# Performance work log

Hardware: AMD Instinct MI355X
Metric: run time of the kernel (lower is better)

## Reference

```python
import jax, jax.numpy as jnp
import numpy as np
import math

B, SL, CH, HZ = 128, 5000, 12, 100
L, D, DFF, H, NC = 5, 1024, 4096, 16, 71
NI = CH * HZ  # 1200
S = SL // HZ  # 50


def setup_inputs() -> dict:
    key = jax.random.key(0)
    ks = jax.random.split(key, 12)
    r = lambda k, shp, sc: jax.random.normal(k, shp, jnp.float32) * sc
    return {
        'x': r(ks[0], (B, SL, CH), 1.0),
        'embed_w': r(ks[1], (NI, D), NI ** -0.5),
        'attn_w': r(ks[2], (L, 4, D, D), D ** -0.5),
        'attn_b': r(ks[3], (L, 4, D), 0.01),
        'ff_w1': r(ks[4], (L, D, DFF), D ** -0.5),
        'ff_b1': r(ks[5], (L, DFF), 0.01),
        'ff_w2': r(ks[6], (L, DFF, D), DFF ** -0.5),
        'ff_b2': r(ks[7], (L, D), 0.01),
        'ln_g': jnp.ones((L, 2, D)), 'ln_b': jnp.zeros((L, 2, D)),
        'fin_g': jnp.ones((D,)), 'fin_b': jnp.zeros((D,)),
        'cf_bn_g': jnp.ones((D,)), 'cf_bn_b': jnp.zeros((D,)),
        'cf_w': r(ks[8], (D, D), D ** -0.5), 'cf_b': r(ks[9], (D,), 0.01),
        'fc_bn_g': jnp.ones((D,)), 'fc_bn_b': jnp.zeros((D,)),
        'fc_w': r(ks[10], (D, NC), D ** -0.5), 'fc_b': r(ks[11], (NC,), 0.01),
    }


def _ln(t, g, b, eps=1e-6):
    # torch LayerNorm variant in source: unbiased std (ddof=1), divide by (std + eps)
    m = t.mean(-1, keepdims=True)
    s = jnp.std(t, axis=-1, ddof=1, keepdims=True)
    return g * (t - m) / (s + eps) + b


def reference(x, embed_w, attn_w, attn_b, ff_w1, ff_b1, ff_w2, ff_b2,
              ln_g, ln_b, fin_g, fin_b, cf_bn_g, cf_bn_b, cf_w, cf_b,
              fc_bn_g, fc_bn_b, fc_w, fc_b):
    Bx, SLx, CHx = x.shape
    Sx = SLx // HZ
    Dx = embed_w.shape[1]
    dk = Dx // H
    # Segmentation (fix): [B, SL, CH] -> [B, S, CH*HZ]; input embed (no bias)
    h = x.reshape(Bx, Sx, CHx * HZ) @ embed_w
    # Positional encoding (sin/cos, detached buffer)
    pos = jnp.arange(Sx, dtype=jnp.float32)[:, None]
    div = jnp.exp(jnp.arange(0, Dx, 2, dtype=jnp.float32) * (-math.log(10000.0) / Dx))
    pe = jnp.zeros((Sx, Dx), jnp.float32)
    pe = pe.at[:, 0::2].set(jnp.sin(pos * div)).at[:, 1::2].set(jnp.cos(pos * div))
    h = h + pe[None]
    # Pre-norm encoder stack (dropout = identity in eval)
    for i in range(attn_w.shape[0]):
        a = _ln(h, ln_g[i, 0], ln_b[i, 0])
        qkv = jnp.einsum('bsd,kde->kbse', a, attn_w[i, :3]) + attn_b[i, :3][:, None, None, :]
        q, k, v = [t.reshape(Bx, Sx, H, dk).transpose(0, 2, 1, 3) for t in qkv]  # bhsd
        sc = jnp.einsum('bhqd,bhkd->bhqk', q, k) / math.sqrt(dk)
        p = jax.nn.softmax(sc, axis=-1)
        o = jnp.einsum('bhqk,bhkd->bhqd', p, v).transpose(0, 2, 1, 3).reshape(Bx, Sx, Dx)
        h = h + o @ attn_w[i, 3] + attn_b[i, 3]
        a2 = _ln(h, ln_g[i, 1], ln_b[i, 1])
        h = h + jax.nn.relu(a2 @ ff_w1[i] + ff_b1[i]) @ ff_w2[i] + ff_b2[i]
    h = _ln(h, fin_g, fin_b)
    # LastPoolRNN(bidirectional=False): last time step
    pooled = h[:, -1, :]
    # BatchNorm1d in eval with running_mean=0, running_var=1
    inv = 1.0 / math.sqrt(1.0 + 1e-5)
    z = (pooled * inv) * cf_bn_g + cf_bn_b
    z = jax.nn.relu(z @ cf_w + cf_b)
    z = (z * inv) * fc_bn_g + fc_bn_b
    return z @ fc_w + fc_b
```

## Files before the change

### kernel.cpp

```cpp
#include <hip/hip_runtime.h>
#include <hip/hip_bf16.h>


typedef __attribute__((ext_vector_type(4))) float f32x4;
typedef __attribute__((ext_vector_type(8))) __bf16 bfvec8;

#define MTOT 6400
#define DMODEL 1024
#define KEMB 1216

__device__ __forceinline__ unsigned short f2bf(float x) {
    __hip_bfloat16 t = __float2bfloat16(x);
    return *reinterpret_cast<unsigned short*>(&t);
}

__device__ __forceinline__ void gl2lds16(const void* g, void* l) {
    __builtin_amdgcn_global_load_lds(
        (__attribute__((address_space(1))) void*)(g),
        (__attribute__((address_space(3))) void*)(l), 16, 0, 0);
}

__global__ __launch_bounds__(256) void tconv(const float* __restrict__ W,
                                             __hip_bfloat16* __restrict__ Wt,
                                             int K, int N, int Kpad) {
    __shared__ float t[32][33];
    const int n0 = blockIdx.x * 32, k0 = blockIdx.y * 32;
    const int tx = threadIdx.x, ty = threadIdx.y;
#pragma unroll
    for (int j = 0; j < 4; ++j) {
        int k = k0 + ty + j * 8, n = n0 + tx;
        float v = (k < K && n < N) ? W[(size_t)k * N + n] : 0.f;
        t[ty + j * 8][tx] = v;
    }
    __syncthreads();
#pragma unroll
    for (int j = 0; j < 4; ++j) {
        int n = n0 + ty + j * 8, k = k0 + tx;
        if (n < N && k < Kpad)
            ((unsigned short*)Wt)[(size_t)n * Kpad + k] = f2bf(t[tx][ty + j * 8]);
    }
}

__global__ __launch_bounds__(256) void xconv(const float* __restrict__ x,
                                             __hip_bfloat16* __restrict__ xb) {
    int q = blockIdx.x * 256 + threadIdx.x;
    if (q >= MTOT * (KEMB / 4)) return;
    int m = q / (KEMB / 4), kq = q - m * (KEMB / 4);
    ushort4 o;
    if (kq < 300) {
        float4 v = reinterpret_cast<const float4*>(x + (size_t)m * 1200)[kq];
        o.x = f2bf(v.x); o.y = f2bf(v.y); o.z = f2bf(v.z); o.w = f2bf(v.w);
    } else { o.x = 0; o.y = 0; o.z = 0; o.w = 0; }
    reinterpret_cast<ushort4*>(xb)[q] = o;
}

__global__ __launch_bounds__(256) void pe_kernel(float* __restrict__ pe) {
    int idx = blockIdx.x * 256 + threadIdx.x;
    if (idx >= 50 * 512) return;
    int s = idx >> 9, i = idx & 511;
    float dv = expf((float)(2 * i) * (-9.210340371976184f / 1024.0f));
    float a = (float)s * dv;
    pe[(s << 10) + 2 * i] = sinf(a);
    pe[(s << 10) + 2 * i + 1] = cosf(a);
}

template<int FLAGS>
__global__ __launch_bounds__(256) void gemm_bt(
                        const __hip_bfloat16* __restrict__ A,
                        const __hip_bfloat16* __restrict__ Bt,
                        float* __restrict__ outF, __hip_bfloat16* __restrict__ outB,
                        const float* __restrict__ bias, const float* __restrict__ res,
                        const float* __restrict__ pe,
                        const float* __restrict__ psg, const float* __restrict__ psb,
                        int M, int N, int K) {
    __shared__ short lds[16384];
    const int tid = threadIdx.x;
    const int w = tid >> 6, l = tid & 63;

    int bx, by;
    {
        const int nwg = gridDim.x * gridDim.y;
        const int wg  = blockIdx.y * gridDim.x + blockIdx.x;
        const int q = nwg >> 3, r = nwg & 7;
        const int xcd = wg & 7, pos = wg >> 3;
        const int nid = (xcd < r) ? xcd * (q + 1) + pos
                                  : r * (q + 1) + (xcd - r) * q + pos;
        by = nid / gridDim.x;
        bx = nid - by * gridDim.x;
    }
    const int row0 = by * 128, col0 = bx * 128;
    const int l15 = l & 15, kof = (l >> 4) << 3;
    const int wr = (w >> 1) << 6, wc = (w & 1) << 6;

    f32x4 acc[4][4];
#pragma unroll
    for (int m = 0; m < 4; ++m)
#pragma unroll
        for (int n = 0; n < 4; ++n) acc[m][n] = (f32x4){0.f, 0.f, 0.f, 0.f};

    int sr[4], sc[4];
#pragma unroll
    for (int c = 0; c < 4; ++c) {
        int e = c * 2048 + w * 512 + l * 8;
        int r = e >> 6;
        int cb = (e & 63) << 1;
        sr[c] = r;
        sc[c] = (cb ^ ((r & 7) << 4)) >> 1;
    }
    const int swz = (l15 & 7) << 4;

    for (int k0 = 0; k0 < K; k0 += 64) {
#pragma unroll
        for (int c = 0; c < 4; ++c)
            gl2lds16(A + (size_t)(row0 + sr[c]) * K + (k0 + sc[c]),
                     &lds[c * 2048 + w * 512]);
#pragma unroll
        for (int c = 0; c < 4; ++c)
            gl2lds16(Bt + (size_t)(col0 + sr[c]) * K + (k0 + sc[c]),
                     &lds[8192 + c * 2048 + w * 512]);
        __syncthreads();
#pragma unroll
        for (int kk = 0; kk < 64; kk += 32) {
            bfvec8 af[4], bfr[4];
#pragma unroll
            for (int m = 0; m < 4; ++m) {
                int r = wr + m * 16 + l15;
                af[m] = *(const bfvec8*)((const char*)lds + r * 128 + ((((kk + kof) << 1)) ^ swz));
            }
#pragma unroll
            for (int n = 0; n < 4; ++n) {
                int r = wc + n * 16 + l15;
                bfr[n] = *(const bfvec8*)((const char*)lds + 16384 + r * 128 + ((((kk + kof) << 1)) ^ swz));
            }
#pragma unroll
            for (int m = 0; m < 4; ++m)
#pragma unroll
                for (int n = 0; n < 4; ++n)
                    acc[m][n] = __builtin_amdgcn_mfma_f32_16x16x32_bf16(af[m], bfr[n], acc[m][n], 0, 0, 0);
        }
        __syncthreads();
    }

    const int rb = row0 + wr + ((l >> 4) << 2);
#pragma unroll
    for (int n = 0; n < 4; ++n) {
        const int cidx = col0 + wc + n * 16 + l15;
        float bv = 0.f, pg = 0.f, pb2 = 0.f;
        if constexpr (FLAGS & 1) bv = bias[cidx];
        if constexpr (FLAGS & 16) {
            pg = 0.99999500003749971f * psg[cidx];
            pb2 = psb[cidx];
        }
#pragma unroll
        for (int m = 0; m < 4; ++m) {
#pragma unroll
            for (int i = 0; i < 4; ++i) {
                int r = rb + m * 16 + i;
                float v = acc[m][n][i] + bv;
                if constexpr (FLAGS & 8) v += pe[(r % 50) * N + cidx];
                if constexpr (FLAGS & 4) v = fmaxf(v, 0.f);
                if constexpr (FLAGS & 2) v += res[(size_t)r * N + cidx];
                if constexpr (FLAGS & 16) v = v * pg + pb2;
                if constexpr (FLAGS & 32) ((unsigned short*)outB)[(size_t)r * N + cidx] = f2bf(v);
                else outF[(size_t)r * N + cidx] = v;
            }
        }
    }
}

__device__ __forceinline__ float wave_sum(float v) {
#pragma unroll
    for (int off = 32; off; off >>= 1) v += __shfl_down(v, off);
    return v;
}

__global__ __launch_bounds__(256) void ln_kernel(const float* __restrict__ h,
                                                 const float* __restrict__ g,
                                                 const float* __restrict__ b,
                                                 __hip_bfloat16* __restrict__ out) {
    const int row = blockIdx.x, tid = threadIdx.x;
    const float4 v = reinterpret_cast<const float4*>(h + (size_t)row * 1024)[tid];
    float s = v.x + v.y + v.z + v.w;
    float s2 = v.x * v.x + v.y * v.y + v.z * v.z + v.w * v.w;
    __shared__ float red[8];
    float ws1 = wave_sum(s), ws2 = wave_sum(s2);
    if ((tid & 63) == 0) { red[tid >> 6] = ws1; red[4 + (tid >> 6)] = ws2; }
    __syncthreads();
    float sum = red[0] + red[1] + red[2] + red[3];
    float sum2 = red[4] + red[5] + red[6] + red[7];
    float mean = sum * (1.f / 1024.f);
    float var = fmaxf(0.f, (sum2 - sum * mean) * (1.f / 1023.f));
    float inv = 1.f / (sqrtf(var) + 1e-6f);
    float4 gv = reinterpret_cast<const float4*>(g)[tid];
    float4 bv = reinterpret_cast<const float4*>(b)[tid];
    ushort4 o;
    o.x = f2bf(gv.x * (v.x - mean) * inv + bv.x);
    o.y = f2bf(gv.y * (v.y - mean) * inv + bv.y);
    o.z = f2bf(gv.z * (v.z - mean) * inv + bv.z);
    o.w = f2bf(gv.w * (v.w - mean) * inv + bv.w);
    reinterpret_cast<ushort4*>(out)[(size_t)row * 256 + tid] = o;
}

__global__ __launch_bounds__(256) void attn_k(const __hip_bfloat16* __restrict__ qkv,
                                              __hip_bfloat16* __restrict__ o) {
    __shared__ float Q[50][66];
    __shared__ float Kk[50][66];
    __shared__ float V[50][66];
    __shared__ float P[50][52];
    const int bid = blockIdx.x;
    const int b = bid >> 4, hh = bid & 15;
    const int tid = threadIdx.x;
    const size_t base0 = (size_t)(b * 50) * 3072 + hh * 64;
    for (int idx = tid; idx < 3200; idx += 256) {
        int s = idx >> 6, d = idx & 63;
        size_t p = base0 + (size_t)s * 3072 + d;
        Q[s][d] = __bfloat162float(qkv[p]);
        Kk[s][d] = __bfloat162float(qkv[p + 1024]);
        V[s][d] = __bfloat162float(qkv[p + 2048]);
    }
    __syncthreads();
    for (int e = tid; e < 2500; e += 256) {
        int i = e / 50, j = e - i * 50;
        float acc = 0.f;
#pragma unroll
        for (int d = 0; d < 64; ++d) acc += Q[i][d] * Kk[j][d];
        P[i][j] = acc * 0.125f;
    }
    __syncthreads();
    if (tid < 50) {
        float mx = -1e30f;
        for (int j = 0; j < 50; ++j) mx = fmaxf(mx, P[tid][j]);
        float sum = 0.f;
        for (int j = 0; j < 50; ++j) { float ev = __expf(P[tid][j] - mx); P[tid][j] = ev; sum += ev; }
        float is = 1.f / sum;
        for (int j = 0; j < 50; ++j) P[tid][j] *= is;
    }
    __syncthreads();
    for (int e = tid; e < 3200; e += 256) {
        int i = e >> 6, d = e & 63;
        float acc = 0.f;
#pragma unroll
        for (int j = 0; j < 50; ++j) acc += P[i][j] * V[j][d];
        o[(size_t)(b * 50 + i) * 1024 + hh * 64 + d] = __float2bfloat16(acc);
    }
}

__global__ __launch_bounds__(256) void pool_kernel(const float* __restrict__ h,
                                                   const float* __restrict__ fg,
                                                   const float* __restrict__ fb,
                                                   const float* __restrict__ cg,
                                                   const float* __restrict__ cb,
                                                   __hip_bfloat16* __restrict__ z) {
    const int bb = blockIdx.x, tid = threadIdx.x;
    const size_t row = (size_t)bb * 50 + 49;
    const float4 v = reinterpret_cast<const float4*>(h + row * 1024)[tid];
    float s = v.x + v.y + v.z + v.w;
    float s2 = v.x * v.x + v.y * v.y + v.z * v.z + v.w * v.w;
    __shared__ float red[8];
    float ws1 = wave_sum(s), ws2 = wave_sum(s2);
    if ((tid & 63) == 0) { red[tid >> 6] = ws1; red[4 + (tid >> 6)] = ws2; }
    __syncthreads();
    float sum = red[0] + red[1] + red[2] + red[3];
    float sum2 = red[4] + red[5] + red[6] + red[7];
    float mean = sum * (1.f / 1024.f);
    float var = fmaxf(0.f, (sum2 - sum * mean) * (1.f / 1023.f));
    float inv = 1.f / (sqrtf(var) + 1e-6f);
    const float INV = 0.99999500003749971f;
    float4 gv = reinterpret_cast<const float4*>(fg)[tid];
    float4 bv = reinterpret_cast<const float4*>(fb)[tid];
    float4 cgv = reinterpret_cast<const float4*>(cg)[tid];
    float4 cbv = reinterpret_cast<const float4*>(cb)[tid];
    ushort4 o;
    o.x = f2bf((gv.x * (v.x - mean) * inv + bv.x) * INV * cgv.x + cbv.x);
    o.y = f2bf((gv.y * (v.y - mean) * inv + bv.y) * INV * cgv.y + cbv.y);
    o.z = f2bf((gv.z * (v.z - mean) * inv + bv.z) * INV * cgv.z + cbv.z);
    o.w = f2bf((gv.w * (v.w - mean) * inv + bv.w) * INV * cgv.w + cbv.w);
    reinterpret_cast<ushort4*>(z)[(size_t)bb * 256 + tid] = o;
}

__global__ __launch_bounds__(128) void fc_kernel(const __hip_bfloat16* __restrict__ z3,
                                                 const float* __restrict__ fw,
                                                 const float* __restrict__ fbias,
                                                 float* __restrict__ out) {
    __shared__ float zr[1024];
    const int b = blockIdx.x, tid = threadIdx.x;
    for (int i = tid; i < 1024; i += 128) zr[i] = __bfloat162float(z3[(size_t)b * 1024 + i]);
    __syncthreads();
    if (tid < 71) {
        float acc = 0.f;
        for (int k = 0; k < 1024; ++k) acc += zr[k] * fw[k * 71 + tid];
        out[b * 71 + tid] = acc + fbias[tid];
    }
}

extern "C" void kernel_launch(void* const* d_in, const int* in_sizes, int n_in,
                              void* d_out, int out_size, void* d_ws, size_t ws_size,
                              hipStream_t stream) {
    const float* x       = (const float*)d_in[0];
    const float* embed_w = (const float*)d_in[1];
    const float* attn_w  = (const float*)d_in[2];
    const float* attn_b  = (const float*)d_in[3];
    const float* ff_w1   = (const float*)d_in[4];
    const float* ff_b1   = (const float*)d_in[5];
    const float* ff_w2   = (const float*)d_in[6];
    const float* ff_b2   = (const float*)d_in[7];
    const float* ln_g    = (const float*)d_in[8];
    const float* ln_b    = (const float*)d_in[9];
    const float* fin_g   = (const float*)d_in[10];
    const float* fin_b   = (const float*)d_in[11];
    const float* cf_bn_g = (const float*)d_in[12];
    const float* cf_bn_b = (const float*)d_in[13];
    const float* cf_w    = (const float*)d_in[14];
    const float* cf_b    = (const float*)d_in[15];
    const float* fc_bn_g = (const float*)d_in[16];
    const float* fc_bn_b = (const float*)d_in[17];
    const float* fc_w    = (const float*)d_in[18];
    const float* fc_b    = (const float*)d_in[19];

    char* ws = (char*)d_ws;
    size_t off = 0;
    auto alloc = [&](size_t bytes) { void* p = ws + off; off += (bytes + 255) & ~(size_t)255; return p; };

    __hip_bfloat16* wbuf = (__hip_bfloat16*)alloc((size_t)12582912 * 2);
    float*          h    = (float*)alloc((size_t)MTOT * DMODEL * 4);
    __hip_bfloat16* abuf = (__hip_bfloat16*)alloc((size_t)MTOT * DMODEL * 2);
    __hip_bfloat16* big  = (__hip_bfloat16*)alloc((size_t)MTOT * 4096 * 2);
    float*          pe   = (float*)alloc((size_t)50 * 1024 * 4);
    __hip_bfloat16* zbuf = (__hip_bfloat16*)alloc((size_t)128 * 1024 * 2);
    __hip_bfloat16* z3   = (__hip_bfloat16*)alloc((size_t)128 * 1024 * 2);

    __hip_bfloat16* qkvT = wbuf;
    __hip_bfloat16* projT = wbuf + (size_t)3072 * 1024;
    __hip_bfloat16* ff1T = wbuf + (size_t)4096 * 1024;
    __hip_bfloat16* ff2T = wbuf + (size_t)8192 * 1024;

    const dim3 tb(32, 8);

    xconv<<<(MTOT * (KEMB / 4) + 255) / 256, 256, 0, stream>>>(x, big);
    pe_kernel<<<100, 256, 0, stream>>>(pe);
    tconv<<<dim3(32, 38), tb, 0, stream>>>(embed_w, wbuf, 1200, 1024, KEMB);
    gemm_bt<8><<<dim3(8, 50), 256, 0, stream>>>(big, wbuf, h, nullptr,
        nullptr, nullptr, pe, nullptr, nullptr, MTOT, DMODEL, KEMB);

    for (int i = 0; i < 5; ++i) {
        for (int k = 0; k < 3; ++k)
            tconv<<<dim3(32, 32), tb, 0, stream>>>(attn_w + ((size_t)i * 4 + k) * 1048576,
                                                   qkvT + (size_t)k * 1048576, 1024, 1024, 1024);
        tconv<<<dim3(32, 32), tb, 0, stream>>>(attn_w + ((size_t)i * 4 + 3) * 1048576,
                                               projT, 1024, 1024, 1024);
        tconv<<<dim3(128, 32), tb, 0, stream>>>(ff_w1 + (size_t)i * 4194304, ff1T, 1024, 4096, 1024);
        tconv<<<dim3(32, 128), tb, 0, stream>>>(ff_w2 + (size_t)i * 4194304, ff2T, 4096, 1024, 4096);

        ln_kernel<<<MTOT, 256, 0, stream>>>(h, ln_g + (size_t)i * 2048, ln_b + (size_t)i * 2048, abuf);
        gemm_bt<33><<<dim3(24, 50), 256, 0, stream>>>(abuf, qkvT, nullptr, big,
            attn_b + (size_t)i * 4096, nullptr, nullptr, nullptr, nullptr, MTOT, 3072, 1024);
        attn_k<<<2048, 256, 0, stream>>>(big, abuf);
        gemm_bt<3><<<dim3(8, 50), 256, 0, stream>>>(abuf, projT, h, nullptr,
            attn_b + (size_t)i * 4096 + 3072, h, nullptr, nullptr, nullptr, MTOT, DMODEL, 1024);
        ln_kernel<<<MTOT, 256, 0, stream>>>(h, ln_g + (size_t)i * 2048 + 1024,
                                            ln_b + (size_t)i * 2048 + 1024, abuf);
        gemm_bt<37><<<dim3(32, 50), 256, 0, stream>>>(abuf, ff1T, nullptr, big,
            ff_b1 + (size_t)i * 4096, nullptr, nullptr, nullptr, nullptr, MTOT, 4096, 1024);
        gemm_bt<3><<<dim3(8, 50), 256, 0, stream>>>(big, ff2T, h, nullptr,
            ff_b2 + (size_t)i * 1024, h, nullptr, nullptr, nullptr, MTOT, DMODEL, 4096);
    }

    pool_kernel<<<128, 256, 0, stream>>>(h, fin_g, fin_b, cf_bn_g, cf_bn_b, zbuf);
    tconv<<<dim3(32, 32), tb, 0, stream>>>(cf_w, wbuf, 1024, 1024, 1024);
    gemm_bt<53><<<dim3(8, 1), 256, 0, stream>>>(zbuf, wbuf, nullptr, z3,
        cf_b, nullptr, nullptr, fc_bn_g, fc_bn_b, 128, 1024, 1024);
    fc_kernel<<<128, 128, 0, stream>>>(z3, fc_w, fc_b, (float*)d_out);

    (void)in_sizes; (void)n_in; (void)out_size; (void)ws_size;
}
```

Before: 2.168 ms.

## Rewrite attention with bf16 MFMA per wave and batch attention weight transposes

Replaces the scalar fp32 LDS attention kernel with one where each wave handles one head. QK^T and PV run on 16x16x32 bf16 MFMA instructions, softmax uses register shuffles, and P and V are staged in padded LDS. The four per-layer attention weight transposes are merged into one launch using a z grid dimension, which cuts launch overhead. P is now rounded to bf16 before the PV product, so there is a small precision change.

New measurement: 1.895 ms. -12.6%, faster.

```diff
diff --git a/kernel.cpp b/kernel.cpp
--- a/kernel.cpp
+++ b/kernel.cpp
@@ -22,14 +22,16 @@
 
 __global__ __launch_bounds__(256) void tconv(const float* __restrict__ W,
                                              __hip_bfloat16* __restrict__ Wt,
-                                             int K, int N, int Kpad) {
+                                             int K, int N, int Kpad, size_t zoff) {
     __shared__ float t[32][33];
+    const float* Wz = W + (size_t)blockIdx.z * zoff;
+    unsigned short* Wtz = (unsigned short*)Wt + (size_t)blockIdx.z * zoff;
     const int n0 = blockIdx.x * 32, k0 = blockIdx.y * 32;
     const int tx = threadIdx.x, ty = threadIdx.y;
 #pragma unroll
     for (int j = 0; j < 4; ++j) {
         int k = k0 + ty + j * 8, n = n0 + tx;
-        float v = (k < K && n < N) ? W[(size_t)k * N + n] : 0.f;
+        float v = (k < K && n < N) ? Wz[(size_t)k * N + n] : 0.f;
         t[ty + j * 8][tx] = v;
     }
     __syncthreads();
@@ -37,7 +39,7 @@
     for (int j = 0; j < 4; ++j) {
         int n = n0 + ty + j * 8, k = k0 + tx;
         if (n < N && k < Kpad)
-            ((unsigned short*)Wt)[(size_t)n * Kpad + k] = f2bf(t[tx][ty + j * 8]);
+            Wtz[(size_t)n * Kpad + k] = f2bf(t[tx][ty + j * 8]);
     }
 }
 
@@ -201,47 +203,125 @@
     reinterpret_cast<ushort4*>(out)[(size_t)row * 256 + tid] = o;
 }
 
-__global__ __launch_bounds__(256) void attn_k(const __hip_bfloat16* __restrict__ qkv,
-                                              __hip_bfloat16* __restrict__ o) {
-    __shared__ float Q[50][66];
-    __shared__ float Kk[50][66];
-    __shared__ float V[50][66];
-    __shared__ float P[50][52];
-    const int bid = blockIdx.x;
-    const int b = bid >> 4, hh = bid & 15;
-    const int tid = threadIdx.x;
-    const size_t base0 = (size_t)(b * 50) * 3072 + hh * 64;
-    for (int idx = tid; idx < 3200; idx += 256) {
-        int s = idx >> 6, d = idx & 63;
-        size_t p = base0 + (size_t)s * 3072 + d;
-        Q[s][d] = __bfloat162float(qkv[p]);
-        Kk[s][d] = __bfloat162float(qkv[p + 1024]);
-        V[s][d] = __bfloat162float(qkv[p + 2048]);
+__global__ __launch_bounds__(128) void attn_mfma(const __hip_bfloat16* __restrict__ qkv,
+                                                 __hip_bfloat16* __restrict__ o) {
+    __shared__ unsigned short plds[2][64 * 72];
+    __shared__ unsigned short vlds[2][64 * 72];
+    const int w = threadIdx.x >> 6, l = threadIdx.x & 63;
+    const int b = blockIdx.x >> 3;
+    const int hh = ((blockIdx.x & 7) << 1) | w;
+    const int l15 = l & 15, g = l >> 4;
+    const size_t rowbase = (size_t)(b * 50) * 3072 + hh * 64;
+
+    {
+        const int j = l;
+        const bool ok = j < 50;
+        const uint4* vp = (const uint4*)(qkv + rowbase + (size_t)j * 3072 + 2048);
+#pragma unroll
+        for (int d8 = 0; d8 < 8; ++d8) {
+            uint4 vv = ok ? vp[d8] : (uint4){0u, 0u, 0u, 0u};
+            const int d0 = d8 * 8;
+            vlds[w][(d0 + 0) * 72 + j] = (unsigned short)(vv.x & 0xffff);
+            vlds[w][(d0 + 1) * 72 + j] = (unsigned short)(vv.x >> 16);
+            vlds[w][(d0 + 2) * 72 + j] = (unsigned short)(vv.y & 0xffff);
+            vlds[w][(d0 + 3) * 72 + j] = (unsigned short)(vv.y >> 16);
+            vlds[w][(d0 + 4) * 72 + j] = (unsigned short)(vv.z & 0xffff);
+            vlds[w][(d0 + 5) * 72 + j] = (unsigned short)(vv.z >> 16);
+            vlds[w][(d0 + 6) * 72 + j] = (unsigned short)(vv.w & 0xffff);
+            vlds[w][(d0 + 7) * 72 + j] = (unsigned short)(vv.w >> 16);
+        }
+    }
+
+    const bfvec8 zf = {};
+    bfvec8 qf[4][2], kf[4][2];
+#pragma unroll
+    for (int mi = 0; mi < 4; ++mi) {
+        const int i = mi * 16 + l15;
+        const bool ok = i < 50;
+        const size_t rq = rowbase + (size_t)i * 3072;
+#pragma unroll
+        for (int ks = 0; ks < 2; ++ks) {
+            const int d = ks * 32 + g * 8;
+            qf[mi][ks] = ok ? *(const bfvec8*)(qkv + rq + d) : zf;
+            kf[mi][ks] = ok ? *(const bfvec8*)(qkv + rq + 1024 + d) : zf;
+        }
+    }
+
+    f32x4 s[4][4];
+#pragma unroll
+    for (int mi = 0; mi < 4; ++mi)
+#pragma unroll
+        for (int nj = 0; nj < 4; ++nj) {
+            s[mi][nj] = (f32x4){0.f, 0.f, 0.f, 0.f};
+#pragma unroll
+            for (int ks = 0; ks < 2; ++ks)
+                s[mi][nj] = __builtin_amdgcn_mfma_f32_16x16x32_bf16(qf[mi][ks], kf[nj][ks], s[mi][nj], 0, 0, 0);
+        }
+
+#pragma unroll
+    for (int mi = 0; mi < 4; ++mi) {
+#pragma unroll
+        for (int r = 0; r < 4; ++r) {
+            const int row = mi * 16 + g * 4 + r;
+            float v[4];
+            float mx = -1e30f;
+#pragma unroll
+            for (int nj = 0; nj < 4; ++nj) {
+                float x = s[mi][nj][r] * 0.125f;
+                if (nj * 16 + l15 >= 50) x = -1e30f;
+                v[nj] = x;
+                mx = fmaxf(mx, x);
+            }
+#pragma unroll
+            for (int m = 1; m < 16; m <<= 1) mx = fmaxf(mx, __shfl_xor(mx, m));
+            float sum = 0.f;
+#pragma unroll
+            for (int nj = 0; nj < 4; ++nj) { v[nj] = __expf(v[nj] - mx); sum += v[nj]; }
+#pragma unroll
+            for (int m = 1; m < 16; m <<= 1) sum += __shfl_xor(sum, m);
+            const float is = 1.f / sum;
+#pragma unroll
+            for (int nj = 0; nj < 4; ++nj)
+                plds[w][row * 72 + nj * 16 + l15] = f2bf(v[nj] * is);
+        }
     }
     __syncthreads();
-    for (int e = tid; e < 2500; e += 256) {
-        int i = e / 50, j = e - i * 50;
-        float acc = 0.f;
-#pragma unroll
-        for (int d = 0; d < 64; ++d) acc += Q[i][d] * Kk[j][d];
-        P[i][j] = acc * 0.125f;
-    }
-    __syncthreads();
-    if (tid < 50) {
-        float mx = -1e30f;
-        for (int j = 0; j < 50; ++j) mx = fmaxf(mx, P[tid][j]);
-        float sum = 0.f;
-        for (int j = 0; j < 50; ++j) { float ev = __expf(P[tid][j] - mx); P[tid][j] = ev; sum += ev; }
-        float is = 1.f / sum;
-        for (int j = 0; j < 50; ++j) P[tid][j] *= is;
-    }
-    __syncthreads();
-    for (int e = tid; e < 3200; e += 256) {
-        int i = e >> 6, d = e & 63;
-        float acc = 0.f;
-#pragma unroll
-        for (int j = 0; j < 50; ++j) acc += P[i][j] * V[j][d];
-        o[(size_t)(b * 50 + i) * 1024 + hh * 64 + d] = __float2bfloat16(acc);
+
+    bfvec8 pa[4][2], vb[4][2];
+#pragma unroll
+    for (int mi = 0; mi < 4; ++mi)
+#pragma unroll
+        for (int ks = 0; ks < 2; ++ks)
+            pa[mi][ks] = *(const bfvec8*)(plds[w] + (mi * 16 + l15) * 72 + ks * 32 + g * 8);
+#pragma unroll
+    for (int dn = 0; dn < 4; ++dn)
+#pragma unroll
+        for (int ks = 0; ks < 2; ++ks)
+            vb[dn][ks] = *(const bfvec8*)(vlds[w] + (dn * 16 + l15) * 72 + ks * 32 + g * 8);
+
+    f32x4 oa[4][4];
+#pragma unroll
+    for (int mi = 0; mi < 4; ++mi)
+#pragma unroll
+        for (int dn = 0; dn < 4; ++dn) {
+            oa[mi][dn] = (f32x4){0.f, 0.f, 0.f, 0.f};
+#pragma unroll
+            for (int ks = 0; ks < 2; ++ks)
+                oa[mi][dn] = __builtin_amdgcn_mfma_f32_16x16x32_bf16(pa[mi][ks], vb[dn][ks], oa[mi][dn], 0, 0, 0);
+        }
+
+#pragma unroll
+    for (int mi = 0; mi < 4; ++mi) {
+#pragma unroll
+        for (int r = 0; r < 4; ++r) {
+            const int i = mi * 16 + g * 4 + r;
+            if (i < 50) {
+                const size_t ob = (size_t)(b * 50 + i) * 1024 + hh * 64;
+#pragma unroll
+                for (int dn = 0; dn < 4; ++dn)
+                    ((unsigned short*)o)[ob + dn * 16 + l15] = f2bf(oa[mi][dn][r]);
+            }
+        }
     }
 }
 
@@ -330,31 +410,28 @@
     __hip_bfloat16* z3   = (__hip_bfloat16*)alloc((size_t)128 * 1024 * 2);
 
     __hip_bfloat16* qkvT = wbuf;
-    __hip_bfloat16* projT = wbuf + (size_t)3072 * 1024;
     __hip_bfloat16* ff1T = wbuf + (size_t)4096 * 1024;
     __hip_bfloat16* ff2T = wbuf + (size_t)8192 * 1024;
+    __hip_bfloat16* projT = wbuf + (size_t)3072 * 1024;
 
     const dim3 tb(32, 8);
 
     xconv<<<(MTOT * (KEMB / 4) + 255) / 256, 256, 0, stream>>>(x, big);
     pe_kernel<<<100, 256, 0, stream>>>(pe);
-    tconv<<<dim3(32, 38), tb, 0, stream>>>(embed_w, wbuf, 1200, 1024, KEMB);
+    tconv<<<dim3(32, 38), tb, 0, stream>>>(embed_w, wbuf, 1200, 1024, KEMB, 0);
     gemm_bt<8><<<dim3(8, 50), 256, 0, stream>>>(big, wbuf, h, nullptr,
         nullptr, nullptr, pe, nullptr, nullptr, MTOT, DMODEL, KEMB);
 
     for (int i = 0; i < 5; ++i) {
-        for (int k = 0; k < 3; ++k)
-            tconv<<<dim3(32, 32), tb, 0, stream>>>(attn_w + ((size_t)i * 4 + k) * 1048576,
-                                                   qkvT + (size_t)k * 1048576, 1024, 1024, 1024);
-        tconv<<<dim3(32, 32), tb, 0, stream>>>(attn_w + ((size_t)i * 4 + 3) * 1048576,
-                                               projT, 1024, 1024, 1024);
-        tconv<<<dim3(128, 32), tb, 0, stream>>>(ff_w1 + (size_t)i * 4194304, ff1T, 1024, 4096, 1024);
-        tconv<<<dim3(32, 128), tb, 0, stream>>>(ff_w2 + (size_t)i * 4194304, ff2T, 4096, 1024, 4096);
+        tconv<<<dim3(32, 32, 4), tb, 0, stream>>>(attn_w + (size_t)i * 4194304,
+                                                  qkvT, 1024, 1024, 1024, 1048576);
+        tconv<<<dim3(128, 32), tb, 0, stream>>>(ff_w1 + (size_t)i * 4194304, ff1T, 1024, 4096, 1024, 0);
+        tconv<<<dim3(32, 128), tb, 0, stream>>>(ff_w2 + (size_t)i * 4194304, ff2T, 4096, 1024, 4096, 0);
 
         ln_kernel<<<MTOT, 256, 0, stream>>>(h, ln_g + (size_t)i * 2048, ln_b + (size_t)i * 2048, abuf);
         gemm_bt<33><<<dim3(24, 50), 256, 0, stream>>>(abuf, qkvT, nullptr, big,
             attn_b + (size_t)i * 4096, nullptr, nullptr, nullptr, nullptr, MTOT, 3072, 1024);
-        attn_k<<<2048, 256, 0, stream>>>(big, abuf);
+        attn_mfma<<<1024, 128, 0, stream>>>(big, abuf);
         gemm_bt<3><<<dim3(8, 50), 256, 0, stream>>>(abuf, projT, h, nullptr,
             attn_b + (size_t)i * 4096 + 3072, h, nullptr, nullptr, nullptr, MTOT, DMODEL, 1024);
         ln_kernel<<<MTOT, 256, 0, stream>>>(h, ln_g + (size_t)i * 2048 + 1024,
@@ -366,7 +443,7 @@
     }
 
     pool_kernel<<<128, 256, 0, stream>>>(h, fin_g, fin_b, cf_bn_g, cf_bn_b, zbuf);
-    tconv<<<dim3(32, 32), tb, 0, stream>>>(cf_w, wbuf, 1024, 1024, 1024);
+    tconv<<<dim3(32, 32), tb, 0, stream>>>(cf_w, wbuf, 1024, 1024, 1024, 0);
     gemm_bt<53><<<dim3(8, 1), 256, 0, stream>>>(zbuf, wbuf, nullptr, z3,
         cf_b, nullptr, nullptr, fc_bn_g, fc_bn_b, 128, 1024, 1024);
     fc_kernel<<<128, 128, 0, stream>>>(z3, fc_w, fc_b, (float*)d_out);
```
